# Kernel optimization log

Measured on AMD Instinct MI355X. Metric: run time of the kernel, lower is better.

Reference implementation:

```python
import jax, jax.numpy as jnp
import numpy as np

N, L, D, ZD, H, C = 128, 256, 256, 128, 8, 32
EPS = 1e-5

def _ln(x, w, b):
    mu = jnp.mean(x, axis=-1, keepdims=True)
    var = jnp.var(x, axis=-1, keepdims=True)
    return (x - mu) * jax.lax.rsqrt(var + EPS) * w + b

def setup_inputs() -> dict:
    key = jax.random.key(0)
    ks = jax.random.split(key, 10)
    s = 0.02
    return {
        "m": jax.random.normal(ks[0], (N, L, D), jnp.float32),
        "z": jax.random.normal(ks[1], (L, L, ZD), jnp.float32),
        "ln1_w": jnp.ones((D,), jnp.float32),
        "ln1_b": jnp.zeros((D,), jnp.float32),
        "wq": jax.random.normal(ks[2], (D, H * C), jnp.float32) * s,
        "wk": jax.random.normal(ks[3], (D, H * C), jnp.float32) * s,
        "wv": jax.random.normal(ks[4], (D, H * C), jnp.float32) * s,
        "lnz_w": jnp.ones((ZD,), jnp.float32),
        "lnz_b": jnp.zeros((ZD,), jnp.float32),
        "wz": jax.random.normal(ks[5], (ZD, H), jnp.float32) * s,
        "wg": jax.random.normal(ks[6], (D, H * C), jnp.float32) * s,
        "bg": jnp.zeros((H * C,), jnp.float32),
        "wo": jax.random.normal(ks[7], (H * C, D), jnp.float32) * s,
        "bo": jnp.zeros((D,), jnp.float32),
    }

def reference(m, z, ln1_w, ln1_b, wq, wk, wv, lnz_w, lnz_b, wz, wg, bg, wo, bo):
    mn = _ln(m, ln1_w, ln1_b)                        # [N,L,D]
    q = (mn @ wq).reshape(N, L, H, C)
    k = (mn @ wk).reshape(N, L, H, C)
    v = (mn @ wv).reshape(N, L, H, C)
    b = _ln(z, lnz_w, lnz_b) @ wz                    # [L,L,H] pair bias
    g = jax.nn.sigmoid(mn @ wg + bg).reshape(N, L, H, C)
    att = jnp.einsum('nqhc,nkhc->nqkh', q, k) * (1.0 / np.sqrt(C)) + b[None]
    att = jax.nn.softmax(att, axis=2)                # over key dim
    o = jnp.einsum('nqkh,nkhc->nqhc', att, v) * g    # gated output
    return o.reshape(N, L, H * C) @ wo + bo          # [N,L,D]
```

## Files before the change

### kernel.cpp

```cpp
#include <hip/hip_runtime.h>
#include <math.h>

typedef unsigned short u16;
typedef unsigned int   u32;
typedef __attribute__((ext_vector_type(8)))  short          bf16x8;
typedef __attribute__((ext_vector_type(4)))  float          f32x4;
typedef __attribute__((ext_vector_type(16))) unsigned short u16x16;

static constexpr int Nn = 128;
static constexpr int Ln = 256;
static constexpr int Dn = 256;
static constexpr int ZDn = 128;
static constexpr int Hn = 8;
static constexpr int Cn = 32;
static constexpr int Mrows = Nn * Ln;
static constexpr float EPS = 1e-5f;
static constexpr float LOG2E = 1.4426950408889634f;
static constexpr int HS = 32768 * 32;

__device__ __forceinline__ float bf_s(u16 u)  { union { u32 i; float f; } x; x.i = ((u32)u) << 16; return x.f; }
__device__ __forceinline__ u32 f2bf(float f) {
  union { float f; u32 i; } x; x.f = f;
  return (x.i + 0x7fffu + ((x.i >> 16) & 1u)) >> 16;
}
__device__ __forceinline__ u32 pk2(float a, float b) { return f2bf(a) | (f2bf(b) << 16); }

__global__ __launch_bounds__(256) void ln_m_kernel(
    const float* __restrict__ x, const float* __restrict__ w,
    const float* __restrict__ b, u16* __restrict__ y)
{
  const int wave = threadIdx.x >> 6;
  const int lane = threadIdx.x & 63;
  const size_t row = (size_t)blockIdx.x * 4 + wave;
  const float4 xv = ((const float4*)(x + row * Dn))[lane];
  float s  = xv.x + xv.y + xv.z + xv.w;
  float s2 = xv.x*xv.x + xv.y*xv.y + xv.z*xv.z + xv.w*xv.w;
  #pragma unroll
  for (int off = 32; off; off >>= 1) {
    s  += __shfl_xor(s, off);
    s2 += __shfl_xor(s2, off);
  }
  const float mu = s * (1.0f / Dn);
  float var = s2 * (1.0f / Dn) - mu * mu;
  var = fmaxf(var, 0.0f);
  const float rstd = rsqrtf(var + EPS);
  const float4 wv = ((const float4*)w)[lane];
  const float4 bv = ((const float4*)b)[lane];
  float4 yv;
  yv.x = (xv.x - mu) * rstd * wv.x + bv.x;
  yv.y = (xv.y - mu) * rstd * wv.y + bv.y;
  yv.z = (xv.z - mu) * rstd * wv.z + bv.z;
  yv.w = (xv.w - mu) * rstd * wv.w + bv.w;
  uint2 p;
  p.x = pk2(yv.x, yv.y);
  p.y = pk2(yv.z, yv.w);
  ((uint2*)(y + row * Dn))[lane] = p;
}

__global__ __launch_bounds__(256) void wcvt_kernel(
    const float* __restrict__ wq, const float* __restrict__ wk,
    const float* __restrict__ wv, const float* __restrict__ wg,
    const float* __restrict__ wo,
    const float* __restrict__ lnz_w, const float* __restrict__ lnz_b,
    const float* __restrict__ wz,
    u16* __restrict__ wcatT, u16* __restrict__ woTh, u16* __restrict__ woTl,
    float* __restrict__ wkhT, float* __restrict__ Sv, float* __restrict__ bsv)
{
  __shared__ float lds[128][8];
  const int bid = blockIdx.x;
  const int t = threadIdx.x;
  if (bid < 1024) {
    const int n = bid & 255, proj = bid >> 8;
    const float* W = proj == 0 ? wq : proj == 1 ? wk : proj == 2 ? wv : wg;
    float v = W[(size_t)t * 256 + n];
    if (proj == 0) v *= 0.17677669529663687f * LOG2E;
    wcatT[(size_t)bid * 256 + t] = (u16)f2bf(v);
  } else if (bid < 1280) {
    const int n = bid - 1024;
    const float x = wo[(size_t)t * 256 + n];
    const u16 h16 = (u16)f2bf(x);
    woTh[(size_t)n * 256 + t] = h16;
    woTl[(size_t)n * 256 + t] = (u16)f2bf(x - bf_s(h16));
  } else {
    if (t < 128) {
      #pragma unroll
      for (int h = 0; h < 8; ++h) {
        const float v = lnz_w[t] * wz[t * 8 + h];
        lds[t][h] = v;
        wkhT[h * 128 + t] = v;
      }
    }
    __syncthreads();
    if (t < 8) {
      float S = 0.0f, bs = 0.0f;
      for (int k = 0; k < 128; ++k) {
        S  += lds[k][t];
        bs += lnz_b[k] * wz[k * 8 + t];
      }
      Sv[t] = S; bsv[t] = LOG2E * bs;
    }
  }
}

__global__ __launch_bounds__(256) void zbias_kernel(
    const float* __restrict__ z, const float* __restrict__ wkhT,
    const float* __restrict__ Sv, const float* __restrict__ bsv,
    float* __restrict__ b2)
{
  __shared__ float zs[64][132];
  __shared__ float wkT_s[8 * 132];
  __shared__ float mu_s[64], rs_s[64];
  const int t = threadIdx.x;
  const int r0 = blockIdx.x * 64;

  #pragma unroll
  for (int u = 0; u < 8; ++u) {
    const int i = u * 256 + t;
    const int row = i >> 5, c4 = i & 31;
    *(float4*)&zs[row][c4 * 4] =
        *(const float4*)(z + (size_t)(r0 + row) * 128 + c4 * 4);
  }
  #pragma unroll
  for (int u = 0; u < 4; ++u) {
    const int i = u * 256 + t;
    wkT_s[(i >> 7) * 132 + (i & 127)] = wkhT[i];
  }
  __syncthreads();

  {
    const int row = t >> 2, q = t & 3;
    float s = 0.0f, s2 = 0.0f;
    #pragma unroll
    for (int u = 0; u < 8; ++u) {
      const float4 v = *(const float4*)&zs[row][(q * 8 + u) * 4];
      s  += v.x + v.y + v.z + v.w;
      s2 += v.x*v.x + v.y*v.y + v.z*v.z + v.w*v.w;
    }
    s += __shfl_xor(s, 1); s2 += __shfl_xor(s2, 1);
    s += __shfl_xor(s, 2); s2 += __shfl_xor(s2, 2);
    if (q == 0) {
      const float mu = s * (1.0f / 128.0f);
      float var = s2 * (1.0f / 128.0f) - mu * mu;
      var = fmaxf(var, 0.0f);
      mu_s[row] = mu;
      rs_s[row] = rsqrtf(var + EPS);
    }
  }
  __syncthreads();

  {
    const int row = t >> 2, hp = t & 3;
    const int h0 = 2 * hp, h1 = 2 * hp + 1;
    float a0 = 0.0f, a1 = 0.0f;
    #pragma unroll
    for (int c4 = 0; c4 < 32; ++c4) {
      const float4 v  = *(const float4*)&zs[row][c4 * 4];
      const float4 w0 = *(const float4*)&wkT_s[h0 * 132 + c4 * 4];
      const float4 w1 = *(const float4*)&wkT_s[h1 * 132 + c4 * 4];
      a0 = fmaf(v.x, w0.x, a0); a0 = fmaf(v.y, w0.y, a0);
      a0 = fmaf(v.z, w0.z, a0); a0 = fmaf(v.w, w0.w, a0);
      a1 = fmaf(v.x, w1.x, a1); a1 = fmaf(v.y, w1.y, a1);
      a1 = fmaf(v.z, w1.z, a1); a1 = fmaf(v.w, w1.w, a1);
    }
    const float mu = mu_s[row];
    const float rs = rs_s[row] * LOG2E;
    const size_t rg = (size_t)(r0 + row);
    b2[(size_t)h0 * 65536 + rg] = rs * (a0 - mu * Sv[h0]) + bsv[h0];
    b2[(size_t)h1 * 65536 + rg] = rs * (a1 - mu * Sv[h1]) + bsv[h1];
  }
}

__global__ __launch_bounds__(256) void mfma_gemm_qkvg(
    const u16* __restrict__ A, const u16* __restrict__ BT,
    u16* __restrict__ qb, u16* __restrict__ kb,
    u16* __restrict__ vb, u16* __restrict__ gb,
    const float* __restrict__ bg)
{
  __shared__ u16 A_s[128 * 32];
  __shared__ u16 B_s[128 * 32];
  const int t  = threadIdx.x;
  const int w  = t >> 6;
  const int lane = t & 63;
  const int g  = lane >> 4;
  const int li = lane & 15;
  const int m0 = blockIdx.x * 128;
  const int n0 = blockIdx.y * 128;
  const int wr = (w & 1) * 64;
  const int wc = (w >> 1) * 64;

  const f32x4 zf = {0.f, 0.f, 0.f, 0.f};
  f32x4 acc[4][4];
  #pragma unroll
  for (int i = 0; i < 4; ++i)
    #pragma unroll
    for (int j = 0; j < 4; ++j) acc[i][j] = zf;

  for (int k0 = 0; k0 < 256; k0 += 32) {
    __syncthreads();
    #pragma unroll
    for (int i = 0; i < 2; ++i) {
      const int cb  = (i*4 + w) * 1024 + lane * 16;
      const int row = cb >> 6;
      const int ku  = (cb & 63) >> 1;
      __builtin_amdgcn_global_load_lds(
          (const __attribute__((address_space(1))) void*)
              (A + (size_t)(m0 + row) * 256 + k0 + ku),
          (__attribute__((address_space(3))) void*)(A_s + (i*4 + w) * 512),
          16, 0, 0);
      __builtin_amdgcn_global_load_lds(
          (const __attribute__((address_space(1))) void*)
              (BT + (size_t)(n0 + row) * 256 + k0 + ku),
          (__attribute__((address_space(3))) void*)(B_s + (i*4 + w) * 512),
          16, 0, 0);
    }
    __syncthreads();
    bf16x8 af[4], bfr[4];
    #pragma unroll
    for (int i = 0; i < 4; ++i)
      af[i] = *(const bf16x8*)&A_s[(wr + i*16 + li) * 32 + g*8];
    #pragma unroll
    for (int j = 0; j < 4; ++j)
      bfr[j] = *(const bf16x8*)&B_s[(wc + j*16 + li) * 32 + g*8];
    #pragma unroll
    for (int i = 0; i < 4; ++i)
      #pragma unroll
      for (int j = 0; j < 4; ++j)
        acc[i][j] = __builtin_amdgcn_mfma_f32_16x16x32_bf16(af[i], bfr[j], acc[i][j], 0, 0, 0);
  }

  #pragma unroll
  for (int j = 0; j < 4; ++j) {
    const int nglob = n0 + wc + j*16 + li;
    const int proj = nglob >> 8;
    const int h    = (nglob >> 5) & 7;
    const int c    = nglob & 31;
    u16* base = proj == 0 ? qb : proj == 1 ? kb : proj == 2 ? vb : gb;
    const float gbias = (proj == 3) ? bg[h*32 + c] : 0.0f;
    #pragma unroll
    for (int i = 0; i < 4; ++i)
      #pragma unroll
      for (int r = 0; r < 4; ++r) {
        const int m = m0 + wr + i*16 + g*4 + r;
        const float v = acc[i][j][r] + gbias;
        base[(size_t)h * HS + (size_t)m * 32 + c] = (u16)f2bf(v);
      }
  }
}

__global__ __launch_bounds__(256) void attn_mfma_kernel(
    const u16* __restrict__ qb, const u16* __restrict__ kb,
    const u16* __restrict__ vb, const u16* __restrict__ gb,
    const float* __restrict__ b2, u16* __restrict__ obuf)
{
  __shared__ u16 VT_s[32 * 264];
  __shared__ u16 P_s[4 * 32 * 72];

  const int h = blockIdx.x;
  const int n = blockIdx.y;
  const int t = threadIdx.x;
  const int w = t >> 6;
  const int lane = t & 63;
  const int g  = lane >> 4;
  const int li = lane & 15;
  const size_t hb = (size_t)h * HS;
  const size_t rowb = (size_t)n * 256;

  {
    const u16* vg = vb + hb + (rowb + t) * 32;
    const u16x16 v0 = *(const u16x16*)vg;
    const u16x16 v1 = *(const u16x16*)(vg + 16);
    #pragma unroll
    for (int c = 0; c < 16; ++c) {
      VT_s[c * 264 + t]        = v0[c];
      VT_s[(c + 16) * 264 + t] = v1[c];
    }
  }

  bf16x8 qfrag[4];
  #pragma unroll
  for (int qt = 0; qt < 4; ++qt)
    qfrag[qt] = *(const bf16x8*)(qb + hb + (rowb + w*64 + qt*16 + li) * 32 + g*8);

  __syncthreads();

  const f32x4 zf = {0.f, 0.f, 0.f, 0.f};
  f32x4 oacc[4][2];
  #pragma unroll
  for (int qt = 0; qt < 4; ++qt) { oacc[qt][0] = zf; oacc[qt][1] = zf; }
  float lpart[4][4] = {};
  const int woff = w * 32 * 72;

  for (int k0 = 0; k0 < 256; k0 += 64) {
    #pragma unroll
    for (int qh = 0; qh < 2; ++qh) {
      #pragma unroll
      for (int kt = 0; kt < 4; ++kt) {
        const int krow = k0 + kt*16 + li;
        const bf16x8 kfrag = *(const bf16x8*)(kb + hb + (rowb + krow) * 32 + g*8);
        #pragma unroll
        for (int qq = 0; qq < 2; ++qq) {
          const int qt = qh*2 + qq;
          f32x4 s = __builtin_amdgcn_mfma_f32_16x16x32_bf16(qfrag[qt], kfrag, zf, 0, 0, 0);
          const int qlo = w*64 + qt*16 + g*4;
          const float* bp = b2 + ((size_t)h << 16) + (size_t)qlo * 256 + (k0 + kt*16 + li);
          #pragma unroll
          for (int r = 0; r < 4; ++r) {
            const float p = __builtin_amdgcn_exp2f(s[r] + bp[(size_t)r * 256]);
            lpart[qt][r] += p;
            P_s[woff + (qq*16 + g*4 + r) * 72 + kt*16 + li] = (u16)f2bf(p);
          }
        }
      }
      __syncthreads();
      #pragma unroll
      for (int ks = 0; ks < 2; ++ks) {
        bf16x8 afr0 = *(const bf16x8*)&P_s[woff + (li)      * 72 + ks*32 + g*8];
        bf16x8 afr1 = *(const bf16x8*)&P_s[woff + (16 + li) * 72 + ks*32 + g*8];
        #pragma unroll
        for (int ct = 0; ct < 2; ++ct) {
          const bf16x8 vfr = *(const bf16x8*)&VT_s[(ct*16 + li) * 264 + k0 + ks*32 + g*8];
          oacc[qh*2+0][ct] = __builtin_amdgcn_mfma_f32_16x16x32_bf16(afr0, vfr, oacc[qh*2+0][ct], 0, 0, 0);
          oacc[qh*2+1][ct] = __builtin_amdgcn_mfma_f32_16x16x32_bf16(afr1, vfr, oacc[qh*2+1][ct], 0, 0, 0);
        }
      }
      __syncthreads();
    }
  }

  #pragma unroll
  for (int qt = 0; qt < 4; ++qt)
    #pragma unroll
    for (int r = 0; r < 4; ++r) {
      float l = lpart[qt][r];
      l += __shfl_xor(l, 1);
      l += __shfl_xor(l, 2);
      l += __shfl_xor(l, 4);
      l += __shfl_xor(l, 8);
      lpart[qt][r] = 1.0f / l;
    }

  #pragma unroll
  for (int qt = 0; qt < 4; ++qt)
    #pragma unroll
    for (int ct = 0; ct < 2; ++ct)
      #pragma unroll
      for (int r = 0; r < 4; ++r) {
        const int q = w*64 + qt*16 + g*4 + r;
        const int c = ct*16 + li;
        const float gpre = bf_s(gb[hb + (rowb + q) * 32 + c]);
        const float gate = 1.0f / (1.0f + __expf(-gpre));
        obuf[(rowb + q) * 256 + h*32 + c] =
            (u16)f2bf(oacc[qt][ct][r] * lpart[qt][r] * gate);
      }
}

__global__ __launch_bounds__(256) void out_proj_kernel(
    const u16* __restrict__ Abuf, const u16* __restrict__ woT,
    const float* __restrict__ bo, float* __restrict__ out)
{
  __shared__ u16 A_s[64 * 264];
  __shared__ u16 B_s[256 * 40];
  const int t  = threadIdx.x;
  const int w  = t >> 6;
  const int lane = t & 63;
  const int g  = lane >> 4;
  const int li = lane & 15;
  const int m0 = blockIdx.x * 64;
  const int wr = (w & 1) * 32;
  const int wc = (w >> 1) * 128;

  #pragma unroll
  for (int j = 0; j < 8; ++j) {
    const int u = j * 256 + t;
    const int row = u >> 5, c8 = u & 31;
    *(uint4*)&A_s[row * 264 + c8 * 8] =
        *(const uint4*)(Abuf + (size_t)(m0 + row) * 256 + c8 * 8);
  }

  const f32x4 zf = {0.f, 0.f, 0.f, 0.f};
  f32x4 acc[2][8];
  #pragma unroll
  for (int i = 0; i < 2; ++i)
    #pragma unroll
    for (int j = 0; j < 8; ++j) acc[i][j] = zf;

  for (int k0 = 0; k0 < 256; k0 += 32) {
    __syncthreads();
    {
      const u16* sh = woT + (size_t)t * 256 + k0;
      #pragma unroll
      for (int u = 0; u < 4; ++u)
        *(uint4*)&B_s[t * 40 + u*8] = *(const uint4*)(sh + u*8);
    }
    __syncthreads();
    bf16x8 af[2];
    #pragma unroll
    for (int i = 0; i < 2; ++i)
      af[i] = *(const bf16x8*)&A_s[(wr + i*16 + li) * 264 + k0 + g*8];
    #pragma unroll
    for (int j = 0; j < 8; ++j) {
      const bf16x8 bfr = *(const bf16x8*)&B_s[(wc + j*16 + li) * 40 + g*8];
      #pragma unroll
      for (int i = 0; i < 2; ++i)
        acc[i][j] = __builtin_amdgcn_mfma_f32_16x16x32_bf16(af[i], bfr, acc[i][j], 0, 0, 0);
    }
  }

  #pragma unroll
  for (int j = 0; j < 8; ++j) {
    const int col = wc + j*16 + li;
    const float bias = bo[col];
    #pragma unroll
    for (int i = 0; i < 2; ++i)
      #pragma unroll
      for (int r = 0; r < 4; ++r) {
        const int m = m0 + wr + i*16 + g*4 + r;
        out[(size_t)m * 256 + col] = acc[i][j][r] + bias;
      }
  }
}

extern "C" void kernel_launch(void* const* d_in, const int* in_sizes, int n_in,
                              void* d_out, int out_size, void* d_ws, size_t ws_size,
                              hipStream_t stream)
{
  const float* m     = (const float*)d_in[0];
  const float* z     = (const float*)d_in[1];
  const float* ln1_w = (const float*)d_in[2];
  const float* ln1_b = (const float*)d_in[3];
  const float* wq    = (const float*)d_in[4];
  const float* wk    = (const float*)d_in[5];
  const float* wv    = (const float*)d_in[6];
  const float* lnz_w = (const float*)d_in[7];
  const float* lnz_b = (const float*)d_in[8];
  const float* wz    = (const float*)d_in[9];
  const float* wg    = (const float*)d_in[10];
  const float* bg    = (const float*)d_in[11];
  const float* wo    = (const float*)d_in[12];
  const float* bo    = (const float*)d_in[13];
  float* out = (float*)d_out;

  char* ws = (char*)d_ws;
  const size_t MB = 1024 * 1024;
  u16*   mn    = (u16*)(ws);
  u16*   qb    = (u16*)(ws + 16*MB);
  u16*   kb    = (u16*)(ws + 32*MB);
  u16*   vb    = (u16*)(ws + 48*MB);
  u16*   gb    = (u16*)(ws + 64*MB);
  float* b2    = (float*)(ws + 80*MB);
  u16*   wcatT = (u16*)(ws + 82*MB);
  u16*   woTh  = (u16*)(ws + 82*MB + 512*1024);
  u16*   woTl  = (u16*)(ws + 82*MB + 640*1024);
  float* wkhT  = (float*)(ws + 82*MB + 768*1024);
  float* Sv    = (float*)(ws + 82*MB + 772*1024);
  float* bsv   = (float*)(ws + 82*MB + 773*1024);
  u16*   obuf  = mn;

  wcvt_kernel<<<1281, 256, 0, stream>>>(wq, wk, wv, wg, wo, lnz_w, lnz_b, wz,
                                        wcatT, woTh, woTl, wkhT, Sv, bsv);
  ln_m_kernel<<<Mrows/4, 256, 0, stream>>>(m, ln1_w, ln1_b, mn);
  zbias_kernel<<<(Ln*Ln)/64, 256, 0, stream>>>(z, wkhT, Sv, bsv, b2);

  mfma_gemm_qkvg<<<dim3(Mrows/128, 1024/128), 256, 0, stream>>>(
      mn, wcatT, qb, kb, vb, gb, bg);

  attn_mfma_kernel<<<dim3(Hn, Nn), 256, 0, stream>>>(qb, kb, vb, gb, b2, obuf);

  out_proj_kernel<<<Mrows/64, 256, 0, stream>>>(obuf, woTh, bo, out);
}
```

Before: 135.4 us.

## Keep softmax probabilities in registers by computing transposed scores in attention

The attention kernel now computes S^T (K as the A operand, Q as B) so each lane's MFMA output rows map straight onto the B-operand layout of a 16x16x16 bf16 MFMA. P can then feed the PV product from registers without a trip through shared memory. This drops the P_s LDS buffer and both __syncthreads per step, vectorizes the bias loads to float4, and vectorizes the gate reads and output writes. The trade-off is more MFMA instructions, since 16x16x16 replaces 16x16x32, plus a dependency on that builtin or inline asm.

```diff
diff --git a/kernel.cpp b/kernel.cpp
--- a/kernel.cpp
+++ b/kernel.cpp
@@ -4,6 +4,7 @@
 typedef unsigned short u16;
 typedef unsigned int   u32;
 typedef __attribute__((ext_vector_type(8)))  short          bf16x8;
+typedef __attribute__((ext_vector_type(4)))  short          bf16x4;
 typedef __attribute__((ext_vector_type(4)))  float          f32x4;
 typedef __attribute__((ext_vector_type(16))) unsigned short u16x16;
 
@@ -19,11 +20,24 @@
 static constexpr int HS = 32768 * 32;
 
 __device__ __forceinline__ float bf_s(u16 u)  { union { u32 i; float f; } x; x.i = ((u32)u) << 16; return x.f; }
+__device__ __forceinline__ float bf_lo(u32 u) { union { u32 i; float f; } x; x.i = u << 16;         return x.f; }
+__device__ __forceinline__ float bf_hi(u32 u) { union { u32 i; float f; } x; x.i = u & 0xffff0000u; return x.f; }
 __device__ __forceinline__ u32 f2bf(float f) {
   union { float f; u32 i; } x; x.f = f;
   return (x.i + 0x7fffu + ((x.i >> 16) & 1u)) >> 16;
 }
 __device__ __forceinline__ u32 pk2(float a, float b) { return f2bf(a) | (f2bf(b) << 16); }
+
+__device__ __forceinline__ f32x4 mfma16(bf16x4 a, bf16x4 b, f32x4 c) {
+#if __has_builtin(__builtin_amdgcn_mfma_f32_16x16x16bf16_1k)
+  return __builtin_amdgcn_mfma_f32_16x16x16bf16_1k(a, b, c, 0, 0, 0);
+#else
+  f32x4 d;
+  asm volatile("v_mfma_f32_16x16x16_bf16 %0, %1, %2, %3"
+               : "=v"(d) : "v"(a), "v"(b), "v"(c));
+  return d;
+#endif
+}
 
 __global__ __launch_bounds__(256) void ln_m_kernel(
     const float* __restrict__ x, const float* __restrict__ w,
@@ -253,7 +267,6 @@
     const float* __restrict__ b2, u16* __restrict__ obuf)
 {
   __shared__ u16 VT_s[32 * 264];
-  __shared__ u16 P_s[4 * 32 * 72];
 
   const int h = blockIdx.x;
   const int n = blockIdx.y;
@@ -287,71 +300,61 @@
   f32x4 oacc[4][2];
   #pragma unroll
   for (int qt = 0; qt < 4; ++qt) { oacc[qt][0] = zf; oacc[qt][1] = zf; }
-  float lpart[4][4] = {};
-  const int woff = w * 32 * 72;
-
-  for (int k0 = 0; k0 < 256; k0 += 64) {
-    #pragma unroll
-    for (int qh = 0; qh < 2; ++qh) {
-      #pragma unroll
-      for (int kt = 0; kt < 4; ++kt) {
-        const int krow = k0 + kt*16 + li;
-        const bf16x8 kfrag = *(const bf16x8*)(kb + hb + (rowb + krow) * 32 + g*8);
-        #pragma unroll
-        for (int qq = 0; qq < 2; ++qq) {
-          const int qt = qh*2 + qq;
-          f32x4 s = __builtin_amdgcn_mfma_f32_16x16x32_bf16(qfrag[qt], kfrag, zf, 0, 0, 0);
-          const int qlo = w*64 + qt*16 + g*4;
-          const float* bp = b2 + ((size_t)h << 16) + (size_t)qlo * 256 + (k0 + kt*16 + li);
-          #pragma unroll
-          for (int r = 0; r < 4; ++r) {
-            const float p = __builtin_amdgcn_exp2f(s[r] + bp[(size_t)r * 256]);
-            lpart[qt][r] += p;
-            P_s[woff + (qq*16 + g*4 + r) * 72 + kt*16 + li] = (u16)f2bf(p);
-          }
-        }
-      }
-      __syncthreads();
-      #pragma unroll
-      for (int ks = 0; ks < 2; ++ks) {
-        bf16x8 afr0 = *(const bf16x8*)&P_s[woff + (li)      * 72 + ks*32 + g*8];
-        bf16x8 afr1 = *(const bf16x8*)&P_s[woff + (16 + li) * 72 + ks*32 + g*8];
-        #pragma unroll
-        for (int ct = 0; ct < 2; ++ct) {
-          const bf16x8 vfr = *(const bf16x8*)&VT_s[(ct*16 + li) * 264 + k0 + ks*32 + g*8];
-          oacc[qh*2+0][ct] = __builtin_amdgcn_mfma_f32_16x16x32_bf16(afr0, vfr, oacc[qh*2+0][ct], 0, 0, 0);
-          oacc[qh*2+1][ct] = __builtin_amdgcn_mfma_f32_16x16x32_bf16(afr1, vfr, oacc[qh*2+1][ct], 0, 0, 0);
-        }
-      }
-      __syncthreads();
-    }
-  }
-
-  #pragma unroll
-  for (int qt = 0; qt < 4; ++qt)
-    #pragma unroll
-    for (int r = 0; r < 4; ++r) {
-      float l = lpart[qt][r];
-      l += __shfl_xor(l, 1);
-      l += __shfl_xor(l, 2);
-      l += __shfl_xor(l, 4);
-      l += __shfl_xor(l, 8);
-      lpart[qt][r] = 1.0f / l;
-    }
-
-  #pragma unroll
-  for (int qt = 0; qt < 4; ++qt)
-    #pragma unroll
-    for (int ct = 0; ct < 2; ++ct)
-      #pragma unroll
-      for (int r = 0; r < 4; ++r) {
-        const int q = w*64 + qt*16 + g*4 + r;
-        const int c = ct*16 + li;
-        const float gpre = bf_s(gb[hb + (rowb + q) * 32 + c]);
-        const float gate = 1.0f / (1.0f + __expf(-gpre));
-        obuf[(rowb + q) * 256 + h*32 + c] =
-            (u16)f2bf(oacc[qt][ct][r] * lpart[qt][r] * gate);
-      }
+  float lpart[4] = {0.f, 0.f, 0.f, 0.f};
+
+  for (int kt = 0; kt < 16; ++kt) {
+    const int krow = kt*16 + li;
+    const bf16x8 kfrag = *(const bf16x8*)(kb + hb + (rowb + krow) * 32 + g*8);
+    const bf16x4 vf0 = *(const bf16x4*)&VT_s[(li)      * 264 + kt*16 + g*4];
+    const bf16x4 vf1 = *(const bf16x4*)&VT_s[(16 + li) * 264 + kt*16 + g*4];
+    #pragma unroll
+    for (int qt = 0; qt < 4; ++qt) {
+      f32x4 s = __builtin_amdgcn_mfma_f32_16x16x32_bf16(kfrag, qfrag[qt], zf, 0, 0, 0);
+      const int q = w*64 + qt*16 + li;
+      const float4 b4 = *(const float4*)(b2 + ((size_t)h << 16) +
+                                         (size_t)q * 256 + kt*16 + g*4);
+      const float p0 = __builtin_amdgcn_exp2f(s[0] + b4.x);
+      const float p1 = __builtin_amdgcn_exp2f(s[1] + b4.y);
+      const float p2 = __builtin_amdgcn_exp2f(s[2] + b4.z);
+      const float p3 = __builtin_amdgcn_exp2f(s[3] + b4.w);
+      lpart[qt] += (p0 + p1) + (p2 + p3);
+      bf16x4 pf;
+      const u32 plo = pk2(p0, p1), phi = pk2(p2, p3);
+      pf[0] = (short)(plo & 0xffff); pf[1] = (short)(plo >> 16);
+      pf[2] = (short)(phi & 0xffff); pf[3] = (short)(phi >> 16);
+      oacc[qt][0] = mfma16(vf0, pf, oacc[qt][0]);
+      oacc[qt][1] = mfma16(vf1, pf, oacc[qt][1]);
+    }
+  }
+
+  float linv[4];
+  #pragma unroll
+  for (int qt = 0; qt < 4; ++qt) {
+    float l = lpart[qt];
+    l += __shfl_xor(l, 16);
+    l += __shfl_xor(l, 32);
+    linv[qt] = 1.0f / l;
+  }
+
+  #pragma unroll
+  for (int qt = 0; qt < 4; ++qt) {
+    const int q = w*64 + qt*16 + li;
+    #pragma unroll
+    for (int ct = 0; ct < 2; ++ct) {
+      const int c0 = ct*16 + g*4;
+      const uint2 gp = *(const uint2*)(gb + hb + (rowb + q) * 32 + c0);
+      const float g0 = 1.0f / (1.0f + __expf(-bf_lo(gp.x)));
+      const float g1 = 1.0f / (1.0f + __expf(-bf_hi(gp.x)));
+      const float g2 = 1.0f / (1.0f + __expf(-bf_lo(gp.y)));
+      const float g3 = 1.0f / (1.0f + __expf(-bf_hi(gp.y)));
+      uint2 r;
+      r.x = pk2(oacc[qt][ct][0] * linv[qt] * g0,
+                oacc[qt][ct][1] * linv[qt] * g1);
+      r.y = pk2(oacc[qt][ct][2] * linv[qt] * g2,
+                oacc[qt][ct][3] * linv[qt] * g3);
+      *(uint2*)(obuf + (rowb + q) * 256 + h*32 + c0) = r;
+    }
+  }
 }
 
 __global__ __launch_bounds__(256) void out_proj_kernel(
```

Measured after the change: 130.5 us. 3.6% less time.
